# Kernel optimization log

Measured on AMD Instinct MI355X. Metric: run time of the kernel, lower is better.

## Reference

```python
import jax, jax.numpy as jnp
import numpy as np

V, E, HD, H, T = 50000, 256, 512, 256, 50  # vocab, embed, hidden_dim, per-direction hidden, tagset
B, S = 128, 512


def setup_inputs() -> dict:
    key = jax.random.key(0)
    ks = jax.random.split(key, 16)
    def n(k, shape, s=0.05):
        return jax.random.normal(k, shape, dtype=jnp.float32) * s
    return {
        "sentences": jax.random.randint(ks[0], (B, S), 0, V),
        "tags": jax.random.randint(ks[1], (B, S), 0, T),
        "mask": jnp.ones((B, S), dtype=bool),
        "embedding": n(ks[2], (V, E), 0.1),
        "w_ih_f": n(ks[3], (4 * H, E)), "w_hh_f": n(ks[4], (4 * H, H)),
        "b_ih_f": n(ks[5], (4 * H,)), "b_hh_f": n(ks[6], (4 * H,)),
        "w_ih_b": n(ks[7], (4 * H, E)), "w_hh_b": n(ks[8], (4 * H, H)),
        "b_ih_b": n(ks[9], (4 * H,)), "b_hh_b": n(ks[10], (4 * H,)),
        "W_out": n(ks[11], (T, HD)), "b_out": n(ks[12], (T,)),
        "start_trans": n(ks[13], (T,), 0.1),
        "end_trans": n(ks[14], (T,), 0.1),
        "trans": n(ks[15], (T, T), 0.1),
    }


def _lstm(xs, w_ih, w_hh, b, reverse):
    # xs: [S, B, E]; PyTorch gate order i, f, g, o
    Hn = w_hh.shape[1]
    def cell(carry, xt):
        h, c = carry
        g = xt @ w_ih.T + h @ w_hh.T + b
        i, f, gg, o = jnp.split(g, 4, axis=-1)
        c = jax.nn.sigmoid(f) * c + jax.nn.sigmoid(i) * jnp.tanh(gg)
        h = jax.nn.sigmoid(o) * jnp.tanh(c)
        return (h, c), h
    z = jnp.zeros((xs.shape[1], Hn), xs.dtype)
    _, hs = jax.lax.scan(cell, (z, z), xs, reverse=reverse)
    return hs  # [S, B, Hn], time-aligned with xs


def reference(sentences, tags, mask, embedding, w_ih_f, w_hh_f, b_ih_f, b_hh_f,
              w_ih_b, w_hh_b, b_ih_b, b_hh_b, W_out, b_out,
              start_trans, end_trans, trans):
    xs = jnp.swapaxes(embedding[sentences], 0, 1)           # [S, B, E]
    hf = _lstm(xs, w_ih_f, w_hh_f, b_ih_f + b_hh_f, False)
    hb = _lstm(xs, w_ih_b, w_hh_b, b_ih_b + b_hh_b, True)
    emis = jnp.concatenate([hf, hb], -1) @ W_out.T + b_out  # [S, B, T]

    tagsT = jnp.swapaxes(tags, 0, 1)                        # [S, B]
    maskT = jnp.swapaxes(mask, 0, 1)                        # [S, B] bool
    mT = maskT.astype(emis.dtype)

    # --- numerator: score of the gold path (first timestep always on, per torchcrf) ---
    emit = jnp.take_along_axis(emis, tagsT[..., None], axis=-1)[..., 0]   # [S, B]
    num = start_trans[tagsT[0]] + emit[0]
    num = num + jnp.sum((trans[tagsT[:-1], tagsT[1:]] + emit[1:]) * mT[1:], axis=0)
    last = jnp.sum(maskT.astype(jnp.int32), axis=0) - 1                    # [B]
    num = num + end_trans[tags[jnp.arange(tags.shape[0]), last]]

    # --- denominator: log-partition via forward algorithm (logsumexp scan) ---
    alpha0 = start_trans[None, :] + emis[0]                 # [B, T]
    def step(alpha, inp):
        e_t, m_t = inp
        nxt = jax.nn.logsumexp(alpha[:, :, None] + trans[None] + e_t[:, None, :], axis=1)
        return jnp.where(m_t[:, None], nxt, alpha), None
    alpha, _ = jax.lax.scan(step, alpha0, (emis[1:], maskT[1:]))
    logZ = jax.nn.logsumexp(alpha + end_trans[None, :], axis=1)

    # model returns -crf(...) with reduction='mean'
    return -jnp.mean(num - logZ)
```

## Files before the change

kernel.cpp:

```cpp
#include <hip/hip_runtime.h>

typedef __bf16 bf16x8 __attribute__((ext_vector_type(8)));
typedef float f32x4 __attribute__((ext_vector_type(4)));
typedef float f32x2 __attribute__((ext_vector_type(2)));
typedef int i32x8 __attribute__((ext_vector_type(8)));
typedef unsigned short ushort_t;
typedef unsigned int u32x4 __attribute__((ext_vector_type(4)));
typedef long i64_t;

constexpr int Ee = 256;
constexpr int HDd = 512;
constexpr int Hh = 256;
constexpr int Tt = 50;
constexpr int Bb = 128;
constexpr int Ss = 512;
constexpr int G4 = 1024;
constexpr int SB = Ss * Bb;
constexpr int Tc = 64;
constexpr int NP = Ss / Tc;
constexpr int HSTR = 272;
constexpr int NSLOT = 16;

constexpr float LOG2E = 1.4426950408889634f;
constexpr float K2f = 2.8853900817779268f;

#define DI __device__ __forceinline__

DI float bf2f(ushort_t u) {
    unsigned int x = ((unsigned int)u) << 16;
    return __builtin_bit_cast(float, x);
}
DI ushort_t f2bf(float f) {
    unsigned int x = __builtin_bit_cast(unsigned int, f);
    x += 0x7fffu + ((x >> 16) & 1u);
    return (ushort_t)(x >> 16);
}
DI bf16x8 cvt8(const float* p) {
    bf16x8 r;
#pragma unroll
    for (int i = 0; i < 8; ++i) r[i] = (__bf16)p[i];
    return r;
}
DI unsigned int pk4_fp8(float a, float b, float c, float d) {
    int v = __builtin_amdgcn_cvt_pk_fp8_f32(a, b, 0, false);
    v = __builtin_amdgcn_cvt_pk_fp8_f32(c, d, v, true);
    return (unsigned int)v;
}
DI unsigned char fp8_1(float a) {
    return (unsigned char)(__builtin_amdgcn_cvt_pk_fp8_f32(a, 0.f, 0, false) & 0xff);
}
DI float rcpf(float x) { return __builtin_amdgcn_rcpf(x); }
DI float rdlane(float v, int l) {
    return __builtin_bit_cast(float, __builtin_amdgcn_readlane(__builtin_bit_cast(int, v), l));
}

#if __has_builtin(__builtin_amdgcn_exp2f)
DI float ex2(float x) { return __builtin_amdgcn_exp2f(x); }
DI float ex2n(float x) { return __builtin_amdgcn_exp2f(-x); }
#else
DI float ex2(float x) {
    float r;
    asm("v_exp_f32 %0, %1\n\ts_nop 0" : "=v"(r) : "v"(x));
    return r;
}
DI float ex2n(float x) {
    float r;
    asm("v_exp_f32 %0, -%1\n\ts_nop 0" : "=v"(r) : "v"(x));
    return r;
}
#endif

DI void lds_barrier() {
    asm volatile("" ::: "memory");
    __builtin_amdgcn_s_waitcnt(0xC07F);
    __builtin_amdgcn_s_barrier();
    asm volatile("" ::: "memory");
}

__global__ void k_prep(const float* __restrict__ wihf, const float* __restrict__ whhf,
                       const float* __restrict__ wihb, const float* __restrict__ whhb,
                       const float* __restrict__ wout,
                       const float* __restrict__ bihf, const float* __restrict__ bhhf,
                       const float* __restrict__ bihb, const float* __restrict__ bhhb,
                       ushort_t* __restrict__ Wihf, ushort_t* __restrict__ Wihb,
                       unsigned char* __restrict__ Whhf8, unsigned char* __restrict__ Whhb8,
                       unsigned char* __restrict__ Wout8,
                       float* __restrict__ biasf, float* __restrict__ biasb,
                       unsigned int* __restrict__ flags) {
    int i = blockIdx.x * 256 + threadIdx.x;
    if (i < G4 * Ee) {
        float s = (((i >> 16) & 3) == 2) ? K2f : LOG2E;
        Wihf[i] = f2bf(wihf[i] * s);
        Wihb[i] = f2bf(wihb[i] * s);
    }
    if (i < G4 * Hh / 4) {
        int base = i * 4;
        float s = (((i >> 14) & 3) == 2) ? K2f : LOG2E;
        ((unsigned int*)Whhf8)[i] = pk4_fp8(whhf[base] * s, whhf[base + 1] * s,
                                            whhf[base + 2] * s, whhf[base + 3] * s);
        ((unsigned int*)Whhb8)[i] = pk4_fp8(whhb[base] * s, whhb[base + 1] * s,
                                            whhb[base + 2] * s, whhb[base + 3] * s);
    }
    if (i < 64 * HDd) Wout8[i] = 0;
    if (i < Tt * HDd) Wout8[i] = fp8_1(wout[i]);
    if (i < G4) {
        float s = (((i >> 8) & 3) == 2) ? K2f : LOG2E;
        biasf[i] = (bihf[i] + bhhf[i]) * s;
        biasb[i] = (bihb[i] + bhhb[i]) * s;
    }
    if (i < 32) flags[i] = 0;
}

struct PhaseArgs {
    const int* sentences;
    const int* tags;
    const float* emb;
    const ushort_t* Wihf;
    const ushort_t* Wihb;
    const float* biasf;
    const float* biasb;
    const unsigned char* Whhf8;
    const unsigned char* Whhb8;
    const unsigned char* Wout8;
    const float* bout;
    const float* start_trans;
    const float* end_trans;
    const float* trans;
    unsigned char* Gbuf;
    unsigned char* Hcat8;
    float* emis;
    float* logZ;
    float* num;
    float* out;
    unsigned int* flags;
};

__global__ __launch_bounds__(512, 2) void k_phase(PhaseArgs a) {
    __shared__ unsigned char hring[NSLOT][16][HSTR];
    const size_t CH = (size_t)Tc * Bb * G4;
    int blk = blockIdx.x;
    int tid = threadIdx.x;

    if (blk < 16) {
        int ln = tid & 15, qd = (tid >> 4) & 3, w = tid >> 6;
        int dir = blk >> 3;
        int b0 = (blk & 7) * 16;
        const unsigned char* Whh8 = dir ? a.Whhb8 : a.Whhf8;
        int jc0 = w * 32 + ln;

        i32x8 wreg[2][4][2];
#pragma unroll
        for (int ct = 0; ct < 2; ++ct)
#pragma unroll
            for (int g = 0; g < 4; ++g) {
                const unsigned char* wb = Whh8 + (size_t)(g * Hh + jc0 + ct * 16) * Hh;
#pragma unroll
                for (int ks = 0; ks < 2; ++ks)
                    wreg[ct][g][ks] = *(const i32x8*)(wb + ks * 128 + qd * 32);
            }
        for (int i = tid; i < NSLOT * 16 * HSTR; i += 512) ((unsigned char*)hring)[i] = 0;
        __syncthreads();
        float creg[2][4] = {};
        int sctr = 0;

        for (int p = 0; p < NP; ++p) {
            if (tid == 0) {
                while (__hip_atomic_load(&a.flags[p], __ATOMIC_RELAXED,
                                         __HIP_MEMORY_SCOPE_AGENT) < 240u)
                    __builtin_amdgcn_s_sleep(1);
                __threadfence();
            }
            __syncthreads();

            const unsigned char* G = a.Gbuf + ((size_t)(dir * 2 + (p & 1))) * CH;
            int goff = ((dir ? (Tc - 1) : 0) * 32 + (b0 >> 2) + qd) * 4096 + jc0 * 16;
            const int gstep = dir ? -(32 * 4096) : (32 * 4096);

            u32x4 guA[2], guB[2];
#pragma unroll
            for (int ct = 0; ct < 2; ++ct)
                guA[ct] = *(const u32x4*)(G + goff + ct * 256);

            auto lstm_step = [&](u32x4(&gcur)[2], u32x4(&gnxt)[2], int step) {
                int rslot = (sctr + NSLOT - 1) & (NSLOT - 1), wslot = sctr & (NSLOT - 1);
                int goff2 = goff + gstep;
                if (step + 1 < Tc) {
#pragma unroll
                    for (int ct = 0; ct < 2; ++ct)
                        gnxt[ct] = *(const u32x4*)(G + goff2 + ct * 256);
                }
                i32x8 av2[2];
#pragma unroll
                for (int ks = 0; ks < 2; ++ks)
                    av2[ks] = *(const i32x8*)&hring[rslot][ln][ks * 128 + qd * 32];
                f32x4 acc[2][4];
#pragma unroll
                for (int ct = 0; ct < 2; ++ct)
#pragma unroll
                    for (int g = 0; g < 4; ++g) {
                        f32x2 lo = __builtin_amdgcn_cvt_pk_f32_fp8((int)gcur[ct][g], false);
                        f32x2 hi = __builtin_amdgcn_cvt_pk_f32_fp8((int)gcur[ct][g], true);
                        acc[ct][g][0] = lo[0];
                        acc[ct][g][1] = lo[1];
                        acc[ct][g][2] = hi[0];
                        acc[ct][g][3] = hi[1];
                    }
#pragma unroll
                for (int ks = 0; ks < 2; ++ks)
#pragma unroll
                    for (int ct = 0; ct < 2; ++ct)
#pragma unroll
                        for (int g = 0; g < 4; ++g)
                            acc[ct][g] = __builtin_amdgcn_mfma_scale_f32_16x16x128_f8f6f4(
                                av2[ks], wreg[ct][g][ks], acc[ct][g],
                                0, 0,
                                0, 127,
                                0, 127);
#pragma unroll
                for (int ct = 0; ct < 2; ++ct)
#pragma unroll
                    for (int reg = 0; reg < 4; ++reg) {
                        float ei = ex2n(acc[ct][0][reg]);
                        float ef = ex2n(acc[ct][1][reg]);
                        float eg = ex2(acc[ct][2][reg]);
                        float eo = ex2n(acc[ct][3][reg]);
                        float pf = 1.f + ef;
                        float pig = (1.f + ei) * (eg + 1.f);
                        float t2 = fmaf(eg, K2f, -K2f);
                        float cn = fmaf(creg[ct][reg], pig, t2 * pf) * rcpf(pf * pig);
                        creg[ct][reg] = cn;
                        float ec = ex2(cn);
                        float h = (ec - 1.f) * rcpf((1.f + eo) * (ec + 1.f));
                        hring[wslot][qd * 4 + reg][jc0 + ct * 16] = fp8_1(h);
                    }
                goff = goff2;
                lds_barrier();

                if ((sctr & 7) == 7) {
                    int tbase = sctr - 7;
                    int rid = tid >> 2;
                    int slotidx = rid >> 4, m = rid & 15;
                    int slot = (tbase + slotidx) & (NSLOT - 1);
                    int qp = tid & 3;
                    int t = dir ? (511 - (tbase + slotidx)) : (tbase + slotidx);
                    const unsigned char* src = &hring[slot][m][qp * 64];
                    unsigned char* dst = a.Hcat8 + ((size_t)(t * Bb + b0 + m)) * HDd + dir * Hh + qp * 64;
#pragma unroll
                    for (int i2 = 0; i2 < 4; ++i2) {
                        u32x4 v;
#pragma unroll
                        for (int k = 0; k < 4; ++k)
                            v[k] = *(const unsigned int*)(src + i2 * 16 + k * 4);
                        *(u32x4*)(dst + i2 * 16) = v;
                    }
                }
                ++sctr;
            };

            for (int step = 0; step < Tc; step += 2) {
                lstm_step(guA, guB, step);
                lstm_step(guB, guA, step + 1);
            }

            __syncthreads();
            if (tid == 0) {
                if (p == NP - 1) __threadfence();
                atomicAdd(&a.flags[8 + p], 1u);
            }
        }
    } else {
        int team = tid >> 8;
        int stid = tid & 255;
        int slot = (blk - 16) * 2 + team;
        int ln = stid & 15, qd = (stid >> 4) & 3, wv = stid >> 6;
        for (int q = 0; q < NP; ++q) {
            if (q >= 2) {
                if (tid == 0)
                    while (__hip_atomic_load(&a.flags[8 + q - 2], __ATOMIC_RELAXED,
                                             __HIP_MEMORY_SCOPE_AGENT) < 16u)
                        __builtin_amdgcn_s_sleep(64);
                __syncthreads();
            }
            for (int tile = slot; tile < 1024; tile += 480) {
                int dir = tile >> 9;
                int rem = tile & 511;
                int rt0 = rem >> 3, ct0 = rem & 7;
                const ushort_t* W = dir ? a.Wihb : a.Wihf;
                const float* bias = dir ? a.biasb : a.biasf;
                unsigned char* Gout = a.Gbuf + ((size_t)(dir * 2 + (q & 1))) * CH;
                int t0 = dir ? (NP - 1 - q) * Tc : q * Tc;
                int r0 = rt0 * 128 + (wv & 1) * 64;
                int n0 = ct0 * 128 + (wv >> 1) * 64;
                const float* aptr[4];
#pragma unroll
                for (int rt = 0; rt < 4; ++rt) {
                    int r = r0 + rt * 16 + ln;
                    int t = t0 + (r >> 7), b = r & 127;
                    aptr[rt] = a.emb + (size_t)a.sentences[b * Ss + t] * Ee;
                }
                int wrow[4];
#pragma unroll
                for (int ct = 0; ct < 4; ++ct) {
                    int c = n0 + ct * 16 + ln;
                    wrow[ct] = (c & 3) * 256 + (c >> 2);
                }
                f32x4 acc[4][4] = {};
                for (int ks = 0; ks < 8; ++ks) {
                    int k0 = ks * 32 + qd * 8;
                    bf16x8 av[4], bfr[4];
#pragma unroll
                    for (int rt = 0; rt < 4; ++rt) av[rt] = cvt8(aptr[rt] + k0);
#pragma unroll
                    for (int ct = 0; ct < 4; ++ct)
                        bfr[ct] = *(const bf16x8*)(W + (size_t)wrow[ct] * Ee + k0);
#pragma unroll
                    for (int rt = 0; rt < 4; ++rt)
#pragma unroll
                        for (int ct = 0; ct < 4; ++ct)
                            acc[rt][ct] = __builtin_amdgcn_mfma_f32_16x16x32_bf16(av[rt], bfr[ct], acc[rt][ct], 0, 0, 0);
                }
#pragma unroll
                for (int rt = 0; rt < 4; ++rt)
#pragma unroll
                    for (int ct = 0; ct < 4; ++ct) {
                        int c = n0 + ct * 16 + ln;
                        float bv = bias[wrow[ct]];
                        unsigned int pk = pk4_fp8(acc[rt][ct][0] + bv, acc[rt][ct][1] + bv,
                                                  acc[rt][ct][2] + bv, acc[rt][ct][3] + bv);
                        int rowq = ((r0 + rt * 16) >> 2) + qd;
                        *(unsigned int*)(Gout + (size_t)rowq * 4096 + (size_t)c * 4) = pk;
                    }
            }
            __syncthreads();
            if (tid == 0) {
                __threadfence();
                atomicAdd(&a.flags[q], 1u);
            }
        }
    }

    if (tid == 0) {
        while (__hip_atomic_load(&a.flags[15], __ATOMIC_RELAXED,
                                 __HIP_MEMORY_SCOPE_AGENT) < 16u)
            __builtin_amdgcn_s_sleep(16);
        __threadfence();
    }
    __syncthreads();
    {
        int ln = tid & 15, qd = (tid >> 4) & 3, w = tid >> 6;
        int r0 = blk * 256 + w * 32;
        f32x4 acc[2][4] = {};
        for (int ks = 0; ks < 16; ++ks) {
            int k0 = ks * 32 + qd * 8;
            i64_t av[2], bfr[4];
#pragma unroll
            for (int rt = 0; rt < 2; ++rt)
                av[rt] = *(const i64_t*)(a.Hcat8 + (size_t)(r0 + rt * 16 + ln) * HDd + k0);
#pragma unroll
            for (int ct = 0; ct < 4; ++ct)
                bfr[ct] = *(const i64_t*)(a.Wout8 + (size_t)(ct * 16 + ln) * HDd + k0);
#pragma unroll
            for (int rt = 0; rt < 2; ++rt)
#pragma unroll
                for (int ct = 0; ct < 4; ++ct)
                    acc[rt][ct] = __builtin_amdgcn_mfma_f32_16x16x32_fp8_fp8(av[rt], bfr[ct], acc[rt][ct], 0, 0, 0);
        }
#pragma unroll
        for (int rt = 0; rt < 2; ++rt)
#pragma unroll
            for (int ct = 0; ct < 4; ++ct) {
                int j = ct * 16 + ln;
                if (j < Tt) {
                    float bv = a.bout[j];
#pragma unroll
                    for (int reg = 0; reg < 4; ++reg) {
                        int row = r0 + rt * 16 + qd * 4 + reg;
                        int t = row >> 7, b = row & 127;
                        a.emis[((size_t)b * Ss + t) * Tt + j] = acc[rt][ct][reg] + bv;
                    }
                }
            }
    }
    __syncthreads();
    if (tid == 0) {
        __threadfence();
        atomicAdd(&a.flags[16], 1u);
        while (__hip_atomic_load(&a.flags[16], __ATOMIC_RELAXED,
                                 __HIP_MEMORY_SCOPE_AGENT) < 256u)
            __builtin_amdgcn_s_sleep(16);
        __threadfence();
    }
    __syncthreads();

    if (blk < 128) {
        if (tid < 64) {
            int j = tid;
            int b = blk;
            const float* eb = a.emis + (size_t)b * Ss * Tt;

            float preg[52];
            preg[50] = 0.f;
            preg[51] = 0.f;
#pragma unroll
            for (int i = 0; i < Tt; ++i)
                preg[i] = (j < Tt) ? __expf(a.trans[i * Tt + j]) : 0.f;

            float astart = (j < Tt) ? (a.start_trans[j] + eb[j]) : 0.f;
            float a0 = __builtin_amdgcn_readfirstlane(astart);
            float vcur = (j < Tt) ? __expf(astart - a0) : 0.f;
            float logacc = a0;

            float ecur[8], enxt[8];
#pragma unroll
            for (int i = 0; i < 8; ++i)
                ecur[i] = (j < Tt && 1 + i < Ss) ? eb[(1 + i) * Tt + j] : 0.f;

            for (int tb = 1; tb < Ss; tb += 8) {
#pragma unroll
                for (int i = 0; i < 8; ++i) {
                    int tn = tb + 8 + i;
                    enxt[i] = (j < Tt && tn < Ss) ? eb[(size_t)tn * Tt + j] : 0.f;
                }
                float ex[8];
#pragma unroll
                for (int i = 0; i < 8; ++i) ex[i] = __expf(ecur[i]);
#pragma unroll
                for (int i = 0; i < 8; ++i) {
                    int t = tb + i;
                    if (t >= Ss) break;
                    float s0 = 0.f, s1 = 0.f, s2 = 0.f, s3 = 0.f;
#pragma unroll
                    for (int i4 = 0; i4 < 13; ++i4) {
                        s0 = fmaf(rdlane(vcur, i4 * 4 + 0), preg[i4 * 4 + 0], s0);
                        s1 = fmaf(rdlane(vcur, i4 * 4 + 1), preg[i4 * 4 + 1], s1);
                        s2 = fmaf(rdlane(vcur, i4 * 4 + 2), preg[i4 * 4 + 2], s2);
                        s3 = fmaf(rdlane(vcur, i4 * 4 + 3), preg[i4 * 4 + 3], s3);
                    }
                    vcur = ((s0 + s1) + (s2 + s3)) * ex[i];
                    if (i == 3) {
                        float n = __builtin_amdgcn_readfirstlane(vcur);
                        vcur *= rcpf(n);
                        logacc += __logf(n);
                    }
                }
                float n = __builtin_amdgcn_readfirstlane(vcur);
                vcur *= rcpf(n);
                logacc += __logf(n);
#pragma unroll
                for (int i = 0; i < 8; ++i) ecur[i] = enxt[i];
            }
            float ve = (j < Tt) ? vcur * __expf(a.end_trans[j]) : 0.f;
            for (int off = 32; off > 0; off >>= 1) ve += __shfl_down(ve, off, 64);
            if (j == 0) a.logZ[b] = logacc + __logf(ve);
        }
    } else {
        float* red = (float*)&hring[1][0][0];
        int b = blk - 128;
        const float* eb = a.emis + (size_t)b * Ss * Tt;
        float v = 0.f;
        int t = 1 + tid;
        if (t < Ss) {
            int tp = a.tags[b * Ss + t - 1], tc = a.tags[b * Ss + t];
            v = a.trans[tp * Tt + tc] + eb[(size_t)t * Tt + tc];
        }
        if (tid == 0) {
            int t0 = a.tags[b * Ss + 0];
            v += a.start_trans[t0] + eb[t0] + a.end_trans[a.tags[b * Ss + Ss - 1]];
        }
        for (int off = 32; off > 0; off >>= 1) v += __shfl_down(v, off, 64);
        if ((tid & 63) == 0) red[tid >> 6] = v;
        __syncthreads();
        if (tid == 0) {
            float s = 0.f;
#pragma unroll
            for (int i = 0; i < 8; ++i) s += red[i];
            a.num[b] = s;
        }
    }
    __syncthreads();
    if (tid == 0) {
        __threadfence();
        atomicAdd(&a.flags[17], 1u);
    }

    if (blk == 0) {
        if (tid == 0) {
            while (__hip_atomic_load(&a.flags[17], __ATOMIC_RELAXED,
                                     __HIP_MEMORY_SCOPE_AGENT) < 256u)
                __builtin_amdgcn_s_sleep(16);
            __threadfence();
        }
        __syncthreads();
        float* red = (float*)&hring[2][0][0];
        float v = (tid < 128) ? (a.num[tid] - a.logZ[tid]) : 0.f;
        for (int off = 32; off > 0; off >>= 1) v += __shfl_down(v, off, 64);
        if ((tid & 63) == 0) red[tid >> 6] = v;
        __syncthreads();
        if (tid == 0) {
            float s = 0.f;
#pragma unroll
            for (int i = 0; i < 8; ++i) s += red[i];
            a.out[0] = -s / 128.f;
        }
    }
}

extern "C" void kernel_launch(void* const* d_in, const int* in_sizes, int n_in,
                              void* d_out, int out_size, void* d_ws, size_t ws_size,
                              hipStream_t stream) {
    const int* sentences = (const int*)d_in[0];
    const int* tags = (const int*)d_in[1];
    const float* emb = (const float*)d_in[3];
    const float* wihf = (const float*)d_in[4];
    const float* whhf = (const float*)d_in[5];
    const float* bihf = (const float*)d_in[6];
    const float* bhhf = (const float*)d_in[7];
    const float* wihb = (const float*)d_in[8];
    const float* whhb = (const float*)d_in[9];
    const float* bihb = (const float*)d_in[10];
    const float* bhhb = (const float*)d_in[11];
    const float* wout = (const float*)d_in[12];
    const float* bout = (const float*)d_in[13];
    const float* start_trans = (const float*)d_in[14];
    const float* end_trans = (const float*)d_in[15];
    const float* trans = (const float*)d_in[16];

    char* ws = (char*)d_ws;
    size_t off = 0;
    auto alloc = [&](size_t bytes) {
        void* p = ws + off;
        off += (bytes + 255) & ~(size_t)255;
        return p;
    };
    ushort_t* Wihf = (ushort_t*)alloc((size_t)G4 * Ee * 2);
    ushort_t* Wihb = (ushort_t*)alloc((size_t)G4 * Ee * 2);
    unsigned char* Whhf8 = (unsigned char*)alloc((size_t)G4 * Hh);
    unsigned char* Whhb8 = (unsigned char*)alloc((size_t)G4 * Hh);
    unsigned char* Wout8 = (unsigned char*)alloc((size_t)64 * HDd);
    float* biasf = (float*)alloc(G4 * 4);
    float* biasb = (float*)alloc(G4 * 4);
    unsigned char* Gbuf = (unsigned char*)alloc((size_t)4 * Tc * Bb * G4);
    unsigned char* Hcat8 = (unsigned char*)alloc((size_t)SB * HDd);
    float* emis = (float*)alloc((size_t)SB * Tt * 4);
    float* logZ = (float*)alloc(Bb * 4);
    float* num = (float*)alloc(Bb * 4);
    unsigned int* flags = (unsigned int*)alloc(64 * 4);
    (void)ws_size; (void)in_sizes; (void)n_in; (void)out_size;

    k_prep<<<dim3((G4 * Ee + 255) / 256), dim3(256), 0, stream>>>(
        wihf, whhf, wihb, whhb, wout, bihf, bhhf, bihb, bhhb,
        Wihf, Wihb, Whhf8, Whhb8, Wout8, biasf, biasb, flags);

    PhaseArgs pa;
    pa.sentences = sentences;
    pa.tags = tags;
    pa.emb = emb;
    pa.Wihf = Wihf;
    pa.Wihb = Wihb;
    pa.biasf = biasf;
    pa.biasb = biasb;
    pa.Whhf8 = Whhf8;
    pa.Whhb8 = Whhb8;
    pa.Wout8 = Wout8;
    pa.bout = bout;
    pa.start_trans = start_trans;
    pa.end_trans = end_trans;
    pa.trans = trans;
    pa.Gbuf = Gbuf;
    pa.Hcat8 = Hcat8;
    pa.emis = emis;
    pa.logZ = logZ;
    pa.num = num;
    pa.out = (float*)d_out;
    pa.flags = flags;

    k_phase<<<dim3(256), dim3(512), 0, stream>>>(pa);
}
```

Measured before the change: 1.249 ms.

## Split CRF forward algorithm into forward and backward halves meeting at midpoint

Measured after the change: 1.200 ms (median of 2 runs). -3.9%, faster.

```diff
diff --git a/kernel.cpp b/kernel.cpp
--- a/kernel.cpp
+++ b/kernel.cpp
@@ -108,7 +108,7 @@
         biasf[i] = (bihf[i] + bhhf[i]) * s;
         biasb[i] = (bihb[i] + bhhb[i]) * s;
     }
-    if (i < 32) flags[i] = 0;
+    if (i < 256) flags[i] = 0;
 }
 
 struct PhaseArgs {
@@ -129,8 +129,10 @@
     unsigned char* Gbuf;
     unsigned char* Hcat8;
     float* emis;
-    float* logZ;
+    float* aC;
+    float* logaccF;
     float* num;
+    float* diffW;
     float* out;
     unsigned int* flags;
 };
@@ -393,9 +395,32 @@
     __syncthreads();
 
     if (blk < 128) {
+        int b = blk;
+        {
+            float* red = (float*)&hring[1][0][0];
+            const float* eb = a.emis + (size_t)b * Ss * Tt;
+            float v = 0.f;
+            int t = 1 + tid;
+            if (t < Ss) {
+                int tp = a.tags[b * Ss + t - 1], tc = a.tags[b * Ss + t];
+                v = a.trans[tp * Tt + tc] + eb[(size_t)t * Tt + tc];
+            }
+            if (tid == 0) {
+                int t0 = a.tags[b * Ss + 0];
+                v += a.start_trans[t0] + eb[t0] + a.end_trans[a.tags[b * Ss + Ss - 1]];
+            }
+            for (int off = 32; off > 0; off >>= 1) v += __shfl_down(v, off, 64);
+            if ((tid & 63) == 0) red[tid >> 6] = v;
+            __syncthreads();
+            if (tid == 0) {
+                float s = 0.f;
+#pragma unroll
+                for (int i = 0; i < 8; ++i) s += red[i];
+                a.num[b] = s;
+            }
+        }
         if (tid < 64) {
             int j = tid;
-            int b = blk;
             const float* eb = a.emis + (size_t)b * Ss * Tt;
 
             float preg[52];
@@ -413,13 +438,13 @@
             float ecur[8], enxt[8];
 #pragma unroll
             for (int i = 0; i < 8; ++i)
-                ecur[i] = (j < Tt && 1 + i < Ss) ? eb[(1 + i) * Tt + j] : 0.f;
-
-            for (int tb = 1; tb < Ss; tb += 8) {
+                ecur[i] = (j < Tt) ? eb[(1 + i) * Tt + j] : 0.f;
+
+            for (int tb = 1; tb < 256; tb += 8) {
 #pragma unroll
                 for (int i = 0; i < 8; ++i) {
                     int tn = tb + 8 + i;
-                    enxt[i] = (j < Tt && tn < Ss) ? eb[(size_t)tn * Tt + j] : 0.f;
+                    enxt[i] = (j < Tt && tn < 256) ? eb[(size_t)tn * Tt + j] : 0.f;
                 }
                 float ex[8];
 #pragma unroll
@@ -427,7 +452,7 @@
 #pragma unroll
                 for (int i = 0; i < 8; ++i) {
                     int t = tb + i;
-                    if (t >= Ss) break;
+                    if (t >= 256) break;
                     float s0 = 0.f, s1 = 0.f, s2 = 0.f, s3 = 0.f;
 #pragma unroll
                     for (int i4 = 0; i4 < 13; ++i4) {
@@ -449,50 +474,106 @@
 #pragma unroll
                 for (int i = 0; i < 8; ++i) ecur[i] = enxt[i];
             }
-            float ve = (j < Tt) ? vcur * __expf(a.end_trans[j]) : 0.f;
-            for (int off = 32; off > 0; off >>= 1) ve += __shfl_down(ve, off, 64);
-            if (j == 0) a.logZ[b] = logacc + __logf(ve);
+            a.aC[b * 64 + j] = vcur;
+            if (j == 0) a.logaccF[b] = logacc;
+            __threadfence();
+            if (j == 0)
+                __hip_atomic_store(&a.flags[32 + b], 1u, __ATOMIC_RELEASE,
+                                   __HIP_MEMORY_SCOPE_AGENT);
         }
     } else {
-        float* red = (float*)&hring[1][0][0];
-        int b = blk - 128;
-        const float* eb = a.emis + (size_t)b * Ss * Tt;
-        float v = 0.f;
-        int t = 1 + tid;
-        if (t < Ss) {
-            int tp = a.tags[b * Ss + t - 1], tc = a.tags[b * Ss + t];
-            v = a.trans[tp * Tt + tc] + eb[(size_t)t * Tt + tc];
-        }
-        if (tid == 0) {
-            int t0 = a.tags[b * Ss + 0];
-            v += a.start_trans[t0] + eb[t0] + a.end_trans[a.tags[b * Ss + Ss - 1]];
-        }
-        for (int off = 32; off > 0; off >>= 1) v += __shfl_down(v, off, 64);
-        if ((tid & 63) == 0) red[tid >> 6] = v;
-        __syncthreads();
-        if (tid == 0) {
-            float s = 0.f;
-#pragma unroll
-            for (int i = 0; i < 8; ++i) s += red[i];
-            a.num[b] = s;
-        }
-    }
-    __syncthreads();
-    if (tid == 0) {
-        __threadfence();
-        atomicAdd(&a.flags[17], 1u);
+        if (tid < 64) {
+            int j = tid;
+            int b = blk - 128;
+            const float* eb = a.emis + (size_t)b * Ss * Tt;
+
+            float pregB[52];
+            pregB[50] = 0.f;
+            pregB[51] = 0.f;
+#pragma unroll
+            for (int i = 0; i < Tt; ++i)
+                pregB[i] = (j < Tt) ? __expf(a.trans[j * Tt + i]) : 0.f;
+
+            float wstart = (j < Tt) ? (eb[(size_t)(Ss - 1) * Tt + j] + a.end_trans[j]) : 0.f;
+            float a0 = __builtin_amdgcn_readfirstlane(wstart);
+            float w = (j < Tt) ? __expf(wstart - a0) : 0.f;
+            float logacc = a0;
+
+            float ecur[8], enxt[8];
+#pragma unroll
+            for (int i = 0; i < 8; ++i)
+                ecur[i] = (j < Tt) ? eb[(size_t)(510 - i) * Tt + j] : 0.f;
+
+            for (int tb = 510; tb >= 256; tb -= 8) {
+#pragma unroll
+                for (int i = 0; i < 8; ++i) {
+                    int tn = tb - 8 - i;
+                    enxt[i] = (j < Tt && tn >= 256) ? eb[(size_t)tn * Tt + j] : 0.f;
+                }
+                float ex[8];
+#pragma unroll
+                for (int i = 0; i < 8; ++i) ex[i] = __expf(ecur[i]);
+#pragma unroll
+                for (int i = 0; i < 8; ++i) {
+                    int t = tb - i;
+                    if (t < 256) break;
+                    float s0 = 0.f, s1 = 0.f, s2 = 0.f, s3 = 0.f;
+#pragma unroll
+                    for (int i4 = 0; i4 < 13; ++i4) {
+                        s0 = fmaf(rdlane(w, i4 * 4 + 0), pregB[i4 * 4 + 0], s0);
+                        s1 = fmaf(rdlane(w, i4 * 4 + 1), pregB[i4 * 4 + 1], s1);
+                        s2 = fmaf(rdlane(w, i4 * 4 + 2), pregB[i4 * 4 + 2], s2);
+                        s3 = fmaf(rdlane(w, i4 * 4 + 3), pregB[i4 * 4 + 3], s3);
+                    }
+                    w = ((s0 + s1) + (s2 + s3)) * ex[i];
+                    if (i == 3) {
+                        float n = __builtin_amdgcn_readfirstlane(w);
+                        w *= rcpf(n);
+                        logacc += __logf(n);
+                    }
+                }
+                float n = __builtin_amdgcn_readfirstlane(w);
+                w *= rcpf(n);
+                logacc += __logf(n);
+#pragma unroll
+                for (int i = 0; i < 8; ++i) ecur[i] = enxt[i];
+            }
+            float s0 = 0.f, s1 = 0.f, s2 = 0.f, s3 = 0.f;
+#pragma unroll
+            for (int i4 = 0; i4 < 13; ++i4) {
+                s0 = fmaf(rdlane(w, i4 * 4 + 0), pregB[i4 * 4 + 0], s0);
+                s1 = fmaf(rdlane(w, i4 * 4 + 1), pregB[i4 * 4 + 1], s1);
+                s2 = fmaf(rdlane(w, i4 * 4 + 2), pregB[i4 * 4 + 2], s2);
+                s3 = fmaf(rdlane(w, i4 * 4 + 3), pregB[i4 * 4 + 3], s3);
+            }
+            float b255 = (s0 + s1) + (s2 + s3);
+
+            while (__hip_atomic_load(&a.flags[32 + b], __ATOMIC_RELAXED,
+                                     __HIP_MEMORY_SCOPE_AGENT) == 0u)
+                __builtin_amdgcn_s_sleep(1);
+            __threadfence();
+            float af = a.aC[b * 64 + j];
+            float d = af * b255;
+            for (int off = 32; off > 0; off >>= 1) d += __shfl_down(d, off, 64);
+            if (j == 0) {
+                float logZ = a.logaccF[b] + logacc + __logf(d);
+                a.diffW[b] = a.num[b] - logZ;
+                __threadfence();
+                atomicAdd(&a.flags[17], 1u);
+            }
+        }
     }
 
     if (blk == 0) {
         if (tid == 0) {
             while (__hip_atomic_load(&a.flags[17], __ATOMIC_RELAXED,
-                                     __HIP_MEMORY_SCOPE_AGENT) < 256u)
+                                     __HIP_MEMORY_SCOPE_AGENT) < 128u)
                 __builtin_amdgcn_s_sleep(16);
             __threadfence();
         }
         __syncthreads();
         float* red = (float*)&hring[2][0][0];
-        float v = (tid < 128) ? (a.num[tid] - a.logZ[tid]) : 0.f;
+        float v = (tid < 128) ? a.diffW[tid] : 0.f;
         for (int off = 32; off > 0; off >>= 1) v += __shfl_down(v, off, 64);
         if ((tid & 63) == 0) red[tid >> 6] = v;
         __syncthreads();
@@ -542,9 +623,11 @@
     unsigned char* Gbuf = (unsigned char*)alloc((size_t)4 * Tc * Bb * G4);
     unsigned char* Hcat8 = (unsigned char*)alloc((size_t)SB * HDd);
     float* emis = (float*)alloc((size_t)SB * Tt * 4);
-    float* logZ = (float*)alloc(Bb * 4);
+    float* aC = (float*)alloc((size_t)Bb * 64 * 4);
+    float* logaccF = (float*)alloc(Bb * 4);
     float* num = (float*)alloc(Bb * 4);
-    unsigned int* flags = (unsigned int*)alloc(64 * 4);
+    float* diffW = (float*)alloc(Bb * 4);
+    unsigned int* flags = (unsigned int*)alloc(1024);
     (void)ws_size; (void)in_sizes; (void)n_in; (void)out_size;
 
     k_prep<<<dim3((G4 * Ee + 255) / 256), dim3(256), 0, stream>>>(
@@ -569,8 +652,10 @@
     pa.Gbuf = Gbuf;
     pa.Hcat8 = Hcat8;
     pa.emis = emis;
-    pa.logZ = logZ;
+    pa.aC = aC;
+    pa.logaccF = logaccF;
     pa.num = num;
+    pa.diffW = diffW;
     pa.out = (float*)d_out;
     pa.flags = flags;
 
```
